# Optimization experiments

Hardware: AMD Instinct MI355X
Metric: run time of the kernel (lower is better)

## Reference

```python
import jax, jax.numpy as jnp
import numpy as np


def _lstm_cell(x, h, c, W_ih, W_hh, b_ih, b_hh):
    # torch gate order: input, forget, cell(g), output
    g = x @ W_ih.T + h @ W_hh.T + b_ih + b_hh
    i, f, gg, o = jnp.split(g, 4, axis=-1)
    c_new = jax.nn.sigmoid(f) * c + jax.nn.sigmoid(i) * jnp.tanh(gg)
    h_new = jax.nn.sigmoid(o) * jnp.tanh(c_new)
    return h_new, c_new


def setup_inputs() -> dict:
    key = jax.random.key(0)
    ks = jax.random.split(key, 11)
    T, B, D, E, H, V = 64, 4096, 32, 32, 5, 10
    IN = D + 3 * E  # 128 = input_size
    s = 0.1
    return {
        "horizon": T,
        "hidden": jax.random.normal(ks[0], (2, B, H), jnp.float32),
        "cell": jax.random.normal(ks[1], (2, B, H), jnp.float32),
        "dec_x": jax.random.normal(ks[2], (T, B, D), jnp.float32),
        "mote_id_cat": jax.random.randint(ks[3], (T, B), 0, V),
        "fault_type_cat": jax.random.randint(ks[4], (T, B), 0, V),
        "mote_fault_cat": jax.random.randint(ks[5], (T, B), 0, V),
        "mote_embed": jax.random.normal(ks[6], (V, E), jnp.float32),
        "W_ih0": jax.random.normal(ks[7], (4 * H, IN), jnp.float32) * s,
        "W_hh0": jax.random.normal(ks[8], (4 * H, H), jnp.float32) * s,
        "b_ih0": jnp.zeros((4 * H,), jnp.float32),
        "b_hh0": jnp.zeros((4 * H,), jnp.float32),
        "W_ih1": jax.random.normal(ks[9], (4 * H, H), jnp.float32) * s,
        "W_hh1": jax.random.normal(ks[10], (4 * H, H), jnp.float32) * s,
        "b_ih1": jnp.zeros((4 * H,), jnp.float32),
        "b_hh1": jnp.zeros((4 * H,), jnp.float32),
    }


def reference(horizon, hidden, cell, dec_x, mote_id_cat, fault_type_cat,
              mote_fault_cat, mote_embed, W_ih0, W_hh0, b_ih0, b_hh0,
              W_ih1, W_hh1, b_ih1, b_hh1):
    # Faithful to source: ALL three categorical features use mote_embed.
    e1 = mote_embed[mote_id_cat]      # [T,B,E]
    e2 = mote_embed[fault_type_cat]   # [T,B,E]
    e3 = mote_embed[mote_fault_cat]   # [T,B,E]
    x = jnp.concatenate([dec_x, e1, e2, e3], axis=-1)[:horizon]  # [T,B,IN]

    # Source re-feeds the SAME initial (hidden, cell) at every horizon step,
    # so steps are independent -> vmap over time (no carried recurrence).
    def step(xt):  # xt: [B, IN]
        h1, _ = _lstm_cell(xt, hidden[0], cell[0], W_ih0, W_hh0, b_ih0, b_hh0)
        h2, _ = _lstm_cell(h1, hidden[1], cell[1], W_ih1, W_hh1, b_ih1, b_hh1)
        return h2  # top-layer output, [B, H]

    return jax.vmap(step)(x)  # [T, B, H]
```

## Files before the change

kernel.cpp:

```cpp
#include <hip/hip_runtime.h>
#include <math.h>

#define HDIM 5
#define GATES 20
#define DDIM 32
#define EDIM 32
#define INDIM 128
#define VOC 10
#define SPN (3 * VOC * GATES)
#define HH_OFF 1024

__device__ __forceinline__ float sigmoidf_(float x) {
    return __builtin_amdgcn_rcpf(1.0f + __expf(-x));
}
__device__ __forceinline__ float tanhf_(float x) {
    float e = __expf(-2.0f * x);
    return fmaf(2.0f, __builtin_amdgcn_rcpf(1.0f + e), -1.0f);
}

__global__ __launch_bounds__(256) void precompute_kernel(
    const float* __restrict__ hidden,
    const float* __restrict__ emb,
    const float* __restrict__ W_ih0,
    const float* __restrict__ W_hh0, const float* __restrict__ b_ih0,
    const float* __restrict__ b_hh0,
    const float* __restrict__ W_hh1, const float* __restrict__ b_ih1,
    const float* __restrict__ b_hh1,
    float* __restrict__ ws, int B)
{
    int gid = blockIdx.x * 256 + threadIdx.x;
    if (gid < SPN) {
        int s = gid / (VOC * GATES);
        int rem = gid % (VOC * GATES);
        int v = rem / GATES, r = rem % GATES;
        const float4* ev = (const float4*)(emb + v * EDIM);
        const float4* wv = (const float4*)(W_ih0 + r * INDIM + DDIM + s * EDIM);
        float a = 0.0f;
        #pragma unroll
        for (int k = 0; k < EDIM / 4; ++k) {
            float4 e4 = ev[k], w4 = wv[k];
            a = fmaf(e4.x, w4.x, a); a = fmaf(e4.y, w4.y, a);
            a = fmaf(e4.z, w4.z, a); a = fmaf(e4.w, w4.w, a);
        }
        ws[gid] = a;
    }
    if (gid < B) {
        float h0[HDIM], h1v[HDIM];
        #pragma unroll
        for (int h = 0; h < HDIM; ++h) {
            h0[h]  = hidden[(size_t)gid * HDIM + h];
            h1v[h] = hidden[((size_t)B + gid) * HDIM + h];
        }
        #pragma unroll
        for (int r = 0; r < GATES; ++r) {
            float a0 = b_ih0[r] + b_hh0[r];
            float a1 = b_ih1[r] + b_hh1[r];
            #pragma unroll
            for (int h = 0; h < HDIM; ++h) {
                a0 = fmaf(h0[h],  W_hh0[r * HDIM + h], a0);
                a1 = fmaf(h1v[h], W_hh1[r * HDIM + h], a1);
            }
            ws[HH_OFF + (size_t)gid * GATES + r] = a0;
            ws[HH_OFF + (size_t)(B + gid) * GATES + r] = a1;
        }
    }
}

__global__ __launch_bounds__(256, 4) void decoder_kernel(
    const float* __restrict__ cell,
    const float* __restrict__ dec_x,
    const int*   __restrict__ midc,
    const int*   __restrict__ ftc,
    const int*   __restrict__ mfc,
    const float* __restrict__ W_ih0,
    const float* __restrict__ W_ih1,
    const float* __restrict__ ws,
    float* __restrict__ out,
    int B, int total)
{
    __shared__ float sP[SPN];
    for (int j = threadIdx.x; j < SPN; j += 256) sP[j] = ws[j];
    __syncthreads();

    const int idx = blockIdx.x * 256 + threadIdx.x;
    if (idx >= total) return;
    const int t = idx / B;
    const int b = idx - t * B;
    (void)t;

    const float4* xp = (const float4*)dec_x + (size_t)idx * (DDIM / 4);
    float4 x[DDIM / 4];
    #pragma unroll
    for (int k = 0; k < DDIM / 4; ++k) x[k] = xp[k];

    const int vm = midc[idx], vf = ftc[idx], vmf = mfc[idx];

    float acc[GATES];
    const float4* hh0p = (const float4*)(ws + HH_OFF + (size_t)b * GATES);
    #pragma unroll
    for (int k = 0; k < 5; ++k) {
        float4 h4 = hh0p[k];
        acc[4 * k + 0] = h4.x; acc[4 * k + 1] = h4.y;
        acc[4 * k + 2] = h4.z; acc[4 * k + 3] = h4.w;
    }

    const float4* P0 = (const float4*)(sP + vm * GATES);
    const float4* P1 = (const float4*)(sP + VOC * GATES + vf * GATES);
    const float4* P2 = (const float4*)(sP + 2 * VOC * GATES + vmf * GATES);
    #pragma unroll
    for (int k = 0; k < 5; ++k) {
        float4 p0 = P0[k], p1 = P1[k], p2 = P2[k];
        acc[4 * k + 0] += p0.x + p1.x + p2.x;
        acc[4 * k + 1] += p0.y + p1.y + p2.y;
        acc[4 * k + 2] += p0.z + p1.z + p2.z;
        acc[4 * k + 3] += p0.w + p1.w + p2.w;
    }

    #pragma unroll
    for (int r = 0; r < GATES; ++r) {
        const float* w = W_ih0 + r * INDIM;
        float a = acc[r];
        #pragma unroll
        for (int k = 0; k < DDIM / 4; ++k) {
            a = fmaf(x[k].x, w[4 * k + 0], a);
            a = fmaf(x[k].y, w[4 * k + 1], a);
            a = fmaf(x[k].z, w[4 * k + 2], a);
            a = fmaf(x[k].w, w[4 * k + 3], a);
        }
        acc[r] = a;
    }

    float h1[HDIM];
    #pragma unroll
    for (int r = 0; r < HDIM; ++r) {
        float c0 = cell[(size_t)b * HDIM + r];
        float ii = sigmoidf_(acc[r]);
        float ff = sigmoidf_(acc[HDIM + r]);
        float gg = tanhf_(acc[2 * HDIM + r]);
        float oo = sigmoidf_(acc[3 * HDIM + r]);
        float cn = fmaf(ff, c0, ii * gg);
        h1[r] = oo * tanhf_(cn);
    }

    float g1[GATES];
    const float4* hh1p = (const float4*)(ws + HH_OFF + (size_t)(B + b) * GATES);
    #pragma unroll
    for (int k = 0; k < 5; ++k) {
        float4 h4 = hh1p[k];
        g1[4 * k + 0] = h4.x; g1[4 * k + 1] = h4.y;
        g1[4 * k + 2] = h4.z; g1[4 * k + 3] = h4.w;
    }
    #pragma unroll
    for (int r = 0; r < GATES; ++r) {
        float a = g1[r];
        #pragma unroll
        for (int h = 0; h < HDIM; ++h)
            a = fmaf(h1[h], W_ih1[r * HDIM + h], a);
        g1[r] = a;
    }

    #pragma unroll
    for (int r = 0; r < HDIM; ++r) {
        float c1 = cell[((size_t)B + b) * HDIM + r];
        float ii = sigmoidf_(g1[r]);
        float ff = sigmoidf_(g1[HDIM + r]);
        float gg = tanhf_(g1[2 * HDIM + r]);
        float oo = sigmoidf_(g1[3 * HDIM + r]);
        float cn = fmaf(ff, c1, ii * gg);
        out[(size_t)idx * HDIM + r] = oo * tanhf_(cn);
    }
}

extern "C" void kernel_launch(void* const* d_in, const int* in_sizes, int n_in,
                              void* d_out, int out_size, void* d_ws, size_t ws_size,
                              hipStream_t stream) {
    const float* hidden = (const float*)d_in[1];
    const float* cellp  = (const float*)d_in[2];
    const float* dec_x  = (const float*)d_in[3];
    const int*   midc   = (const int*)d_in[4];
    const int*   ftc    = (const int*)d_in[5];
    const int*   mfc    = (const int*)d_in[6];
    const float* emb    = (const float*)d_in[7];
    const float* W_ih0  = (const float*)d_in[8];
    const float* W_hh0  = (const float*)d_in[9];
    const float* b_ih0  = (const float*)d_in[10];
    const float* b_hh0  = (const float*)d_in[11];
    const float* W_ih1  = (const float*)d_in[12];
    const float* W_hh1  = (const float*)d_in[13];
    const float* b_ih1  = (const float*)d_in[14];
    const float* b_hh1  = (const float*)d_in[15];
    float* out = (float*)d_out;
    float* ws  = (float*)d_ws;

    int B = in_sizes[1] / (2 * HDIM);
    int horizon = out_size / (B * HDIM);
    int total = horizon * B;

    int pre_n = (B > SPN ? B : SPN);
    int pre_grid = (pre_n + 255) / 256;
    precompute_kernel<<<pre_grid, 256, 0, stream>>>(
        hidden, emb, W_ih0, W_hh0, b_ih0, b_hh0, W_hh1, b_ih1, b_hh1, ws, B);

    int grid = (total + 255) / 256;
    if (grid < 1) grid = 1;
    decoder_kernel<<<grid, 256, 0, stream>>>(
        cellp, dec_x, midc, ftc, mfc, W_ih0, W_ih1, ws, out, B, total);
}
```

Measured before the change: 119.2 us.

## Transpose hidden-gate workspace to gate-major and drop shared-memory table staging

The precomputed per-batch hidden contributions are stored gate-major ([gate][B]), so each gate load across a wavefront is coalesced instead of a strided float4 per thread. The embedding projection table is read straight from global memory (cached) instead of being staged into LDS with a block barrier. The launch becomes a 2D grid over (batch, time), which removes the integer divide. The trade-off is 40 scalar loads per thread instead of 10 float4 loads, and table lookups go through the cache instead of LDS.

```diff
diff --git a/kernel.cpp b/kernel.cpp
--- a/kernel.cpp
+++ b/kernel.cpp
@@ -60,8 +60,8 @@
                 a0 = fmaf(h0[h],  W_hh0[r * HDIM + h], a0);
                 a1 = fmaf(h1v[h], W_hh1[r * HDIM + h], a1);
             }
-            ws[HH_OFF + (size_t)gid * GATES + r] = a0;
-            ws[HH_OFF + (size_t)(B + gid) * GATES + r] = a1;
+            ws[HH_OFF + (size_t)r * B + gid] = a0;
+            ws[HH_OFF + (size_t)(GATES + r) * B + gid] = a1;
         }
     }
 }
@@ -76,19 +76,14 @@
     const float* __restrict__ W_ih1,
     const float* __restrict__ ws,
     float* __restrict__ out,
-    int B, int total)
+    int B)
 {
-    __shared__ float sP[SPN];
-    for (int j = threadIdx.x; j < SPN; j += 256) sP[j] = ws[j];
-    __syncthreads();
+    const int b = blockIdx.x * 256 + threadIdx.x;
+    if (b >= B) return;
+    const int t = blockIdx.y;
+    const size_t idx = (size_t)t * B + b;
 
-    const int idx = blockIdx.x * 256 + threadIdx.x;
-    if (idx >= total) return;
-    const int t = idx / B;
-    const int b = idx - t * B;
-    (void)t;
-
-    const float4* xp = (const float4*)dec_x + (size_t)idx * (DDIM / 4);
+    const float4* xp = (const float4*)(dec_x + idx * DDIM);
     float4 x[DDIM / 4];
     #pragma unroll
     for (int k = 0; k < DDIM / 4; ++k) x[k] = xp[k];
@@ -96,17 +91,13 @@
     const int vm = midc[idx], vf = ftc[idx], vmf = mfc[idx];
 
     float acc[GATES];
-    const float4* hh0p = (const float4*)(ws + HH_OFF + (size_t)b * GATES);
+    const float* hh0 = ws + HH_OFF;
     #pragma unroll
-    for (int k = 0; k < 5; ++k) {
-        float4 h4 = hh0p[k];
-        acc[4 * k + 0] = h4.x; acc[4 * k + 1] = h4.y;
-        acc[4 * k + 2] = h4.z; acc[4 * k + 3] = h4.w;
-    }
+    for (int r = 0; r < GATES; ++r) acc[r] = hh0[(size_t)r * B + b];
 
-    const float4* P0 = (const float4*)(sP + vm * GATES);
-    const float4* P1 = (const float4*)(sP + VOC * GATES + vf * GATES);
-    const float4* P2 = (const float4*)(sP + 2 * VOC * GATES + vmf * GATES);
+    const float4* P0 = (const float4*)(ws + vm * GATES);
+    const float4* P1 = (const float4*)(ws + VOC * GATES + vf * GATES);
+    const float4* P2 = (const float4*)(ws + 2 * VOC * GATES + vmf * GATES);
     #pragma unroll
     for (int k = 0; k < 5; ++k) {
         float4 p0 = P0[k], p1 = P1[k], p2 = P2[k];
@@ -143,16 +134,10 @@
     }
 
     float g1[GATES];
-    const float4* hh1p = (const float4*)(ws + HH_OFF + (size_t)(B + b) * GATES);
-    #pragma unroll
-    for (int k = 0; k < 5; ++k) {
-        float4 h4 = hh1p[k];
-        g1[4 * k + 0] = h4.x; g1[4 * k + 1] = h4.y;
-        g1[4 * k + 2] = h4.z; g1[4 * k + 3] = h4.w;
-    }
+    const float* hh1 = ws + HH_OFF + (size_t)GATES * B;
     #pragma unroll
     for (int r = 0; r < GATES; ++r) {
-        float a = g1[r];
+        float a = hh1[(size_t)r * B + b];
         #pragma unroll
         for (int h = 0; h < HDIM; ++h)
             a = fmaf(h1[h], W_ih1[r * HDIM + h], a);
@@ -167,7 +152,7 @@
         float gg = tanhf_(g1[2 * HDIM + r]);
         float oo = sigmoidf_(g1[3 * HDIM + r]);
         float cn = fmaf(ff, c1, ii * gg);
-        out[(size_t)idx * HDIM + r] = oo * tanhf_(cn);
+        out[idx * HDIM + r] = oo * tanhf_(cn);
     }
 }
 
@@ -194,15 +179,13 @@
 
     int B = in_sizes[1] / (2 * HDIM);
     int horizon = out_size / (B * HDIM);
-    int total = horizon * B;
 
     int pre_n = (B > SPN ? B : SPN);
     int pre_grid = (pre_n + 255) / 256;
     precompute_kernel<<<pre_grid, 256, 0, stream>>>(
         hidden, emb, W_ih0, W_hh0, b_ih0, b_hh0, W_hh1, b_ih1, b_hh1, ws, B);
 
-    int grid = (total + 255) / 256;
-    if (grid < 1) grid = 1;
+    dim3 grid((B + 255) / 256, horizon, 1);
     decoder_kernel<<<grid, 256, 0, stream>>>(
-        cellp, dec_x, midc, ftc, mfc, W_ih0, W_ih1, ws, out, B, total);
+        cellp, dec_x, midc, ftc, mfc, W_ih0, W_ih1, ws, out, B);
 }
```

New measurement: 121.3 us. Within noise of the previous version (+1.8%).
